# Kernel optimization log

Measured on AMD Instinct MI355X. Metric: run time of the kernel, lower is better.

The kernel has to match this reference:

```python
import jax, jax.numpy as jnp
import numpy as np

NODE_CNT = 1_000_000
EMB_DIM = 128     # embedding_dim
H1 = 128          # hidden_dim_list[1] (leaf fc, linear, no bias)
H0 = 128          # hidden_dim_list[0] (root fc, sigmoid, bias)
B, N0, N1 = 1024, 25, 10


def setup_inputs() -> dict:
    key = jax.random.key(0)
    k1, k2, k3, k4, k5, k6, k7 = jax.random.split(key, 7)
    roots = jax.random.randint(k1, (B,), 0, NODE_CNT)
    idx1 = jax.random.randint(k2, (B, N0), 0, NODE_CNT)
    idx2 = jax.random.randint(k3, (B, N0, N1), 0, NODE_CNT)
    embed_table = jax.random.normal(k4, (NODE_CNT + 1, EMB_DIM), dtype=jnp.float32) * 0.05
    # fc1: last layer, input 2*EMB_DIM -> H1, no bias, linear
    W1 = jax.random.normal(k5, (2 * EMB_DIM, H1), dtype=jnp.float32) * 0.05
    # fc0: input EMB_DIM + H1 -> H0, bias, sigmoid
    W0 = jax.random.normal(k6, (EMB_DIM + H1, H0), dtype=jnp.float32) * 0.05
    b0 = jax.random.normal(k7, (H0,), dtype=jnp.float32) * 0.05
    return {"embed_table": embed_table, "W0": W0, "b0": b0, "W1": W1,
            "roots": roots, "idx1": idx1, "idx2": idx2}


def reference(embed_table, W0, b0, W1, roots, idx1, idx2):
    # Layer 1 (leaf): mean of sampled 2-hop neighbor embeddings
    leaf = embed_table[idx2]                      # [B, N0, N1, D]
    mean_leaf = jnp.mean(leaf, axis=-2)           # [B, N0, D]
    h1 = embed_table[idx1]                        # [B, N0, D]
    z1 = jnp.concatenate([h1, mean_leaf], axis=-1) @ W1   # [B, N0, H1] (linear, no bias)
    # Layer 0 (root): mean of layer-1 outputs over first-hop neighbors
    mean0 = jnp.mean(z1, axis=1)                  # [B, H1]
    h0 = embed_table[roots]                       # [B, D]
    out = jax.nn.sigmoid(jnp.concatenate([h0, mean0], axis=-1) @ W0 + b0)  # [B, H0]
    return out
```

## Files before the change

### kernel.cpp

```cpp
#include <hip/hip_runtime.h>

#define NBATCH 1024
#define N0     25
#define N1     10
#define NLEAF  (N0 * N1)

__global__ __launch_bounds__(256) void sage_fused(
    const float* __restrict__ emb,
    const float* __restrict__ W0,
    const float* __restrict__ b0,
    const float* __restrict__ W1,
    const int* __restrict__ roots,
    const int* __restrict__ idx1,
    const int* __restrict__ idx2,
    float* __restrict__ out)
{
    const int b    = blockIdx.x;
    const int tid  = threadIdx.x;
    const int slot = tid >> 4;
    const int cc   = tid & 15;

    __shared__ int   sidx2[NLEAF];
    __shared__ int   sidx1[N0];
    __shared__ float red[16][128];
    __shared__ float hr[128];
    __shared__ float m1[128];
    __shared__ float m2[128];
    __shared__ float tv[128];
    __shared__ int   sroot;

    if (tid < NLEAF) sidx2[tid] = idx2[b * NLEAF + tid];
    if (tid >= 231)  sidx1[tid - 231] = idx1[b * N0 + (tid - 231)];
    if (tid == 0)    sroot = roots[b];
    __syncthreads();

    const float4* embq = (const float4*)emb;

    float acc[8];
#pragma unroll
    for (int j = 0; j < 8; ++j) acc[j] = 0.f;
#pragma unroll 5
    for (int i = 0; i < 15; ++i) {
        int id = sidx2[slot + 16 * i];
        const float4* p = embq + (size_t)id * 32 + cc * 2;
        float4 v0 = p[0];
        float4 v1 = p[1];
        acc[0] += v0.x; acc[1] += v0.y; acc[2] += v0.z; acc[3] += v0.w;
        acc[4] += v1.x; acc[5] += v1.y; acc[6] += v1.z; acc[7] += v1.w;
    }
    if (slot < 10) {
        int id = sidx2[slot + 240];
        const float4* p = embq + (size_t)id * 32 + cc * 2;
        float4 v0 = p[0];
        float4 v1 = p[1];
        acc[0] += v0.x; acc[1] += v0.y; acc[2] += v0.z; acc[3] += v0.w;
        acc[4] += v1.x; acc[5] += v1.y; acc[6] += v1.z; acc[7] += v1.w;
    }
#pragma unroll
    for (int j = 0; j < 8; ++j) red[slot][cc * 8 + j] = acc[j];
    __syncthreads();
    if (tid < 128) {
        float s = 0.f;
#pragma unroll
        for (int g = 0; g < 16; ++g) s += red[g][tid];
        m2[tid] = s * (1.0f / NLEAF);
    }
    __syncthreads();

#pragma unroll
    for (int j = 0; j < 8; ++j) acc[j] = 0.f;
    {
        int id = sidx1[slot];
        const float4* p = embq + (size_t)id * 32 + cc * 2;
        float4 v0 = p[0];
        float4 v1 = p[1];
        acc[0] += v0.x; acc[1] += v0.y; acc[2] += v0.z; acc[3] += v0.w;
        acc[4] += v1.x; acc[5] += v1.y; acc[6] += v1.z; acc[7] += v1.w;
    }
    if (slot < 9) {
        int id = sidx1[slot + 16];
        const float4* p = embq + (size_t)id * 32 + cc * 2;
        float4 v0 = p[0];
        float4 v1 = p[1];
        acc[0] += v0.x; acc[1] += v0.y; acc[2] += v0.z; acc[3] += v0.w;
        acc[4] += v1.x; acc[5] += v1.y; acc[6] += v1.z; acc[7] += v1.w;
    } else if (slot == 15) {
        const float4* p = embq + (size_t)sroot * 32 + cc * 2;
        float4 v0 = p[0];
        float4 v1 = p[1];
        hr[cc * 8 + 0] = v0.x; hr[cc * 8 + 1] = v0.y;
        hr[cc * 8 + 2] = v0.z; hr[cc * 8 + 3] = v0.w;
        hr[cc * 8 + 4] = v1.x; hr[cc * 8 + 5] = v1.y;
        hr[cc * 8 + 6] = v1.z; hr[cc * 8 + 7] = v1.w;
    }
#pragma unroll
    for (int j = 0; j < 8; ++j) red[slot][cc * 8 + j] = acc[j];
    __syncthreads();
    if (tid < 128) {
        float s = 0.f;
#pragma unroll
        for (int g = 0; g < 16; ++g) s += red[g][tid];
        m1[tid] = s * (1.0f / N0);
    }
    __syncthreads();

    const int c = tid & 127;
    const int h = tid >> 7;
    {
        const float* xh = h ? m2 : m1;
        const float* w = W1 + (size_t)(h * 128) * 128 + c;
        float p = 0.f;
#pragma unroll 8
        for (int k = 0; k < 128; ++k) {
            p += xh[k] * w[(size_t)k * 128];
        }
        red[h][c] = p;
    }
    __syncthreads();
    if (tid < 128) tv[tid] = red[0][tid] + red[1][tid];
    __syncthreads();

    {
        const float* yh = h ? tv : hr;
        const float* w = W0 + (size_t)(h * 128) * 128 + c;
        float q = 0.f;
#pragma unroll 8
        for (int k = 0; k < 128; ++k) {
            q += yh[k] * w[(size_t)k * 128];
        }
        red[h][c] = q;
    }
    __syncthreads();
    if (tid < 128) {
        float z = red[0][tid] + red[1][tid] + b0[tid];
        float s = 1.0f / (1.0f + __expf(-z));
        out[(size_t)b * 128 + tid] = s;
    }
}

extern "C" void kernel_launch(void* const* d_in, const int* in_sizes, int n_in,
                              void* d_out, int out_size, void* d_ws, size_t ws_size,
                              hipStream_t stream) {
    const float* emb   = (const float*)d_in[0];
    const float* W0    = (const float*)d_in[1];
    const float* b0    = (const float*)d_in[2];
    const float* W1    = (const float*)d_in[3];
    const int*   roots = (const int*)d_in[4];
    const int*   idx1  = (const int*)d_in[5];
    const int*   idx2  = (const int*)d_in[6];
    float* out = (float*)d_out;

    sage_fused<<<NBATCH, 256, 0, stream>>>(emb, W0, b0, W1, roots, idx1, idx2, out);
}
```

Baseline: 590.2 us.

## Split gather across four blocks per batch row and add a separate finish kernel

Splits the fused kernel into a gather kernel that launches four blocks per batch row. Each block sums a quarter of the leaf and first-hop embeddings and writes partial sums to workspace. A second kernel reduces the partials, loads the root embedding and runs the two small matmuls with the sigmoid. The aim is more blocks in flight to hide random-gather latency across the GPU, at the cost of an extra launch and a workspace round trip. Byte offsets are now computed with 32-bit arithmetic; the emb table is about 512 MB, so these offsets still fit.

```diff
diff --git a/kernel.cpp b/kernel.cpp
--- a/kernel.cpp
+++ b/kernel.cpp
@@ -4,53 +4,52 @@
 #define N0     25
 #define N1     10
 #define NLEAF  (N0 * N1)
+#define SPLITS 4
 
-__global__ __launch_bounds__(256) void sage_fused(
+__global__ __launch_bounds__(256) void sage_gather(
     const float* __restrict__ emb,
-    const float* __restrict__ W0,
-    const float* __restrict__ b0,
-    const float* __restrict__ W1,
-    const int* __restrict__ roots,
     const int* __restrict__ idx1,
     const int* __restrict__ idx2,
-    float* __restrict__ out)
+    float* __restrict__ ws)
 {
-    const int b    = blockIdx.x;
+    const int blk  = blockIdx.x;
+    const int b    = blk >> 2;
+    const int s    = blk & 3;
     const int tid  = threadIdx.x;
     const int slot = tid >> 4;
     const int cc   = tid & 15;
 
-    __shared__ int   sidx2[NLEAF];
-    __shared__ int   sidx1[N0];
+    const int lstart = s * 63;
+    const int lcnt   = (s == 3) ? (NLEAF - 3 * 63) : 63;
+    const int istart = s * 7;
+    const int icnt   = (s == 3) ? (N0 - 3 * 7) : 7;
+
+    __shared__ int   sidx[80];
     __shared__ float red[16][128];
-    __shared__ float hr[128];
-    __shared__ float m1[128];
-    __shared__ float m2[128];
-    __shared__ float tv[128];
-    __shared__ int   sroot;
 
-    if (tid < NLEAF) sidx2[tid] = idx2[b * NLEAF + tid];
-    if (tid >= 231)  sidx1[tid - 231] = idx1[b * N0 + (tid - 231)];
-    if (tid == 0)    sroot = roots[b];
+    if (tid < lcnt)                   sidx[tid]      = idx2[b * NLEAF + lstart + tid];
+    if (tid >= 64 && tid < 64 + icnt) sidx[tid]      = idx1[b * N0 + istart + (tid - 64)];
     __syncthreads();
 
-    const float4* embq = (const float4*)emb;
+    const char* embb = (const char*)emb;
+    const uint32_t coff = (uint32_t)cc * 32u;
 
     float acc[8];
 #pragma unroll
     for (int j = 0; j < 8; ++j) acc[j] = 0.f;
-#pragma unroll 5
-    for (int i = 0; i < 15; ++i) {
-        int id = sidx2[slot + 16 * i];
-        const float4* p = embq + (size_t)id * 32 + cc * 2;
+
+#pragma unroll
+    for (int i = 0; i < 3; ++i) {
+        int id = sidx[slot + 16 * i];
+        const float4* p = (const float4*)(embb + (uint32_t)id * 512u + coff);
         float4 v0 = p[0];
         float4 v1 = p[1];
         acc[0] += v0.x; acc[1] += v0.y; acc[2] += v0.z; acc[3] += v0.w;
         acc[4] += v1.x; acc[5] += v1.y; acc[6] += v1.z; acc[7] += v1.w;
     }
-    if (slot < 10) {
-        int id = sidx2[slot + 240];
-        const float4* p = embq + (size_t)id * 32 + cc * 2;
+    if (slot + 48 < lcnt) {
+        int id = sidx[slot + 48];
+        const float4* p = (const float4*)(embb + (uint32_t)id * 512u + coff);
         float4 v0 = p[0];
         float4 v1 = p[1];
         acc[0] += v0.x; acc[1] += v0.y; acc[2] += v0.z; acc[3] += v0.w;
@@ -60,64 +59,82 @@
     for (int j = 0; j < 8; ++j) red[slot][cc * 8 + j] = acc[j];
     __syncthreads();
     if (tid < 128) {
-        float s = 0.f;
+        float t = 0.f;
 #pragma unroll
-        for (int g = 0; g < 16; ++g) s += red[g][tid];
-        m2[tid] = s * (1.0f / NLEAF);
+        for (int g = 0; g < 16; ++g) t += red[g][tid];
+        ws[(size_t)blk * 256 + tid] = t;
     }
     __syncthreads();
 
 #pragma unroll
     for (int j = 0; j < 8; ++j) acc[j] = 0.f;
-    {
-        int id = sidx1[slot];
-        const float4* p = embq + (size_t)id * 32 + cc * 2;
+    if (slot < icnt) {
+        int id = sidx[64 + slot];
+        const float4* p = (const float4*)(embb + (uint32_t)id * 512u + coff);
         float4 v0 = p[0];
         float4 v1 = p[1];
         acc[0] += v0.x; acc[1] += v0.y; acc[2] += v0.z; acc[3] += v0.w;
         acc[4] += v1.x; acc[5] += v1.y; acc[6] += v1.z; acc[7] += v1.w;
     }
-    if (slot < 9) {
-        int id = sidx1[slot + 16];
-        const float4* p = embq + (size_t)id * 32 + cc * 2;
-        float4 v0 = p[0];
-        float4 v1 = p[1];
-        acc[0] += v0.x; acc[1] += v0.y; acc[2] += v0.z; acc[3] += v0.w;
-        acc[4] += v1.x; acc[5] += v1.y; acc[6] += v1.z; acc[7] += v1.w;
-    } else if (slot == 15) {
-        const float4* p = embq + (size_t)sroot * 32 + cc * 2;
-        float4 v0 = p[0];
-        float4 v1 = p[1];
-        hr[cc * 8 + 0] = v0.x; hr[cc * 8 + 1] = v0.y;
-        hr[cc * 8 + 2] = v0.z; hr[cc * 8 + 3] = v0.w;
-        hr[cc * 8 + 4] = v1.x; hr[cc * 8 + 5] = v1.y;
-        hr[cc * 8 + 6] = v1.z; hr[cc * 8 + 7] = v1.w;
-    }
 #pragma unroll
     for (int j = 0; j < 8; ++j) red[slot][cc * 8 + j] = acc[j];
     __syncthreads();
     if (tid < 128) {
-        float s = 0.f;
+        float t = 0.f;
 #pragma unroll
-        for (int g = 0; g < 16; ++g) s += red[g][tid];
-        m1[tid] = s * (1.0f / N0);
+        for (int g = 0; g < 16; ++g) t += red[g][tid];
+        ws[(size_t)blk * 256 + 128 + tid] = t;
+    }
+}
+
+__global__ __launch_bounds__(256) void sage_finish(
+    const float* __restrict__ emb,
+    const float* __restrict__ W0,
+    const float* __restrict__ b0,
+    const float* __restrict__ W1,
+    const int* __restrict__ roots,
+    const float* __restrict__ ws,
+    float* __restrict__ out)
+{
+    const int b   = blockIdx.x;
+    const int tid = threadIdx.x;
+
+    __shared__ float hr[128];
+    __shared__ float m1[128];
+    __shared__ float m2[128];
+    __shared__ float tv[128];
+    __shared__ float red2[2][128];
+
+    const int root = roots[b];
+    if (tid < 32) {
+        float4 v = ((const float4*)((const char*)emb + (uint32_t)root * 512u))[tid];
+        ((float4*)hr)[tid] = v;
+    }
+
+    {
+        float p = 0.f;
+#pragma unroll
+        for (int s = 0; s < SPLITS; ++s) p += ws[(size_t)b * 1024 + s * 256 + tid];
+        if (tid < 128) m2[tid] = p * (1.0f / NLEAF);
+        else           m1[tid - 128] = p * (1.0f / N0);
     }
     __syncthreads();
 
     const int c = tid & 127;
     const int h = tid >> 7;
+
     {
         const float* xh = h ? m2 : m1;
         const float* w = W1 + (size_t)(h * 128) * 128 + c;
-        float p = 0.f;
+        float q = 0.f;
 #pragma unroll 8
         for (int k = 0; k < 128; ++k) {
-            p += xh[k] * w[(size_t)k * 128];
+            q += xh[k] * w[(size_t)k * 128];
         }
-        red[h][c] = p;
+        red2[h][c] = q;
     }
     __syncthreads();
-    if (tid < 128) tv[tid] = red[0][tid] + red[1][tid];
+    if (tid < 128) tv[tid] = red2[0][tid] + red2[1][tid];
     __syncthreads();
 
     {
@@ -128,13 +145,13 @@
         for (int k = 0; k < 128; ++k) {
             q += yh[k] * w[(size_t)k * 128];
         }
-        red[h][c] = q;
+        red2[h][c] = q;
     }
     __syncthreads();
     if (tid < 128) {
-        float z = red[0][tid] + red[1][tid] + b0[tid];
-        float s = 1.0f / (1.0f + __expf(-z));
-        out[(size_t)b * 128 + tid] = s;
+        float z = red2[0][tid] + red2[1][tid] + b0[tid];
+        float sg = 1.0f / (1.0f + __expf(-z));
+        out[(size_t)b * 128 + tid] = sg;
     }
 }
 
@@ -149,6 +166,8 @@
     const int*   idx1  = (const int*)d_in[5];
     const int*   idx2  = (const int*)d_in[6];
     float* out = (float*)d_out;
+    float* ws  = (float*)d_ws;
 
-    sage_fused<<<NBATCH, 256, 0, stream>>>(emb, W0, b0, W1, roots, idx1, idx2, out);
+    sage_gather<<<NBATCH * SPLITS, 256, 0, stream>>>(emb, idx1, idx2, ws);
+    sage_finish<<<NBATCH, 256, 0, stream>>>(emb, W0, b0, W1, roots, ws, out);
 }
```

After: 598.8 us. No clear change (+1.5%).
